# Optimization experiments

Measured on AMD Instinct MI355X. Metric: run time of the kernel, lower is better.

## Reference

```python
import jax, jax.numpy as jnp
import numpy as np

# ---- fixed architecture constants (from init_kwargs) ----
N_WALL, N_ROOF, N_WINDOW = 4, 1, 2
N_RC = N_WALL + N_ROOF
HID = 32
ENC_LEN = 48
DT = 900.0
R_OPAQUE, C_OPAQUE = 10.0, 1.0e5
R_TRANS = 2.0
DIRECT_COEF, ABS_WALL_COEF, ABS_ROOF_COEF = 0.5, 0.5, 0.5
C_ZONE = 1.0e5
B, T = 2048, 1440


def setup_inputs() -> dict:
    key = jax.random.key(0)
    k0, k1, k2 = jax.random.split(key, 3)
    input_X = jax.random.normal(k0, (B, T, 7), dtype=jnp.float32)
    # EnvelopeRC deterministic inits
    rc_R_inv = jnp.concatenate([
        1.0 / (10.0 + 1.0 * jnp.arange(N_WALL, dtype=jnp.float32)),
        1.0 / (20.0 + 2.0 * jnp.arange(N_ROOF, dtype=jnp.float32))])
    rc_C_inv = jnp.concatenate([
        1.0 / (80.0 + 10.0 * jnp.arange(N_WALL, dtype=jnp.float32)),
        1.0 / (60.0 + 10.0 * jnp.arange(N_ROOF, dtype=jnp.float32))])
    window_R_inv = 1.0 / (1.0 + 0.1 * jnp.arange(N_WINDOW, dtype=jnp.float32))
    # Internal MLP: xavier_uniform with gain 0.1, zero bias
    lim1 = 0.1 * np.sqrt(6.0 / (2 + HID))
    int_W1 = jax.random.uniform(k1, (HID, 2), jnp.float32, -lim1, lim1)
    int_b1 = jnp.zeros((HID,), jnp.float32)
    lim2 = 0.1 * np.sqrt(6.0 / (HID + 1))
    int_W2 = jax.random.uniform(k2, (1, HID), jnp.float32, -lim2, lim2)
    int_b2 = jnp.zeros((1,), jnp.float32)
    return {
        'input_X': input_X,
        'rc_R_inv': rc_R_inv, 'rc_C_inv': rc_C_inv, 'window_R_inv': window_R_inv,
        'hvac_gain': jnp.float32(0.1),
        'int_W1': int_W1, 'int_b1': int_b1, 'int_W2': int_W2, 'int_b2': int_b2,
        'int_gain': jnp.float32(0.1),
        'direct_gain': jnp.float32(0.1), 'abs_wall': jnp.float32(0.1), 'abs_roof': jnp.float32(0.1),
        'zone_C_inv': jnp.float32(1.0 / 10000.0),
    }


def _forward(input_X, rc_R_inv, rc_C_inv, window_R_inv, hvac_gain,
             int_W1, int_b1, int_W2, int_b2, int_gain,
             direct_gain, abs_wall, abs_roof, zone_C_inv):
    sp = jax.nn.softplus
    Bn, Tn = input_X.shape[0], input_X.shape[1]
    tz_gt  = input_X[:, :, 0]   # [B,T]
    t_amb  = input_X[:, :, 1]
    sol    = input_X[:, :, 2]
    int_x  = input_X[:, :, 3:6]
    hvac_x = input_X[:, :, 6]

    # Internal MLP (state-free -> vectorized over time)
    h1  = jax.nn.relu(jnp.einsum('bti,hi->bth', int_x[:, :, :2], int_W1) + int_b1)
    sch = jax.nn.sigmoid(jnp.einsum('bth,oh->bto', h1, int_W2) + int_b2)[:, :, 0] + int_x[:, :, 2]
    q_int  = sp(int_gain) * 0.1 * sch          # [B,T]
    q_hvac = sp(hvac_gain) * 0.1 * hvac_x      # [B,T]

    # Bounded RC parameters
    r_inv   = sp(rc_R_inv) * (1.0 / R_OPAQUE)  # [n_rc]
    c_inv   = sp(rc_C_inv) * (1.0 / C_OPAQUE)  # [n_rc]
    win_rsum = jnp.sum(sp(window_R_inv)) * (1.0 / R_TRANS)
    abs_rc  = jnp.where(jnp.arange(N_RC) < N_WALL,
                        sp(abs_wall) * ABS_WALL_COEF,
                        sp(abs_roof) * ABS_ROOF_COEF)   # [n_rc]
    q_dir   = sp(direct_gain) * DIRECT_COEF * sol       # [B,T]
    cz_inv  = sp(zone_C_inv) * (1.0 / C_ZONE)

    # Initial state: Tmid_i = 0.7*Tzone0 + 0.3*Tamb0
    Tz0   = tz_gt[:, 0]                                      # [B]
    Tmid0 = jnp.broadcast_to((0.7 * Tz0 + 0.3 * t_amb[:, 0])[:, None], (Bn, N_RC))

    # Teacher forcing during encoder window: carry GT zone temp while t+1 < enc_len
    tz_gt_next = jnp.concatenate([tz_gt[:, 1:], tz_gt[:, -1:]], axis=1)  # [B,T]
    use_gt = (jnp.arange(Tn) + 1) < ENC_LEN                              # [T]

    xs = (t_amb.T, sol.T, q_dir.T, q_int.T, q_hvac.T, tz_gt_next.T, use_gt)

    def step(carry, x):
        Tz, Tmid = carry                      # [B], [B,n_rc]
        ta, so, qd, qi, qh, gt_next, ug = x
        q_in  = (ta[:, None] - Tmid) * r_inv
        q_out = (Tmid - Tz[:, None]) * r_inv
        dTmid = (q_in - q_out + so[:, None] * abs_rc) * c_inv
        q_env = jnp.sum(q_out, axis=1) + (ta - Tz) * win_rsum
        dTz   = (q_env + qi + qh + qd) * cz_inv
        Tz_new   = Tz + dTz * DT
        Tmid_new = Tmid + dTmid * DT
        Tz_carry = jnp.where(ug, gt_next, Tz_new)
        return (Tz_carry, Tmid_new), Tz_new

    _, tz_seq = jax.lax.scan(step, (Tz0, Tmid0), xs)   # [T,B]
    return jnp.transpose(tz_seq)[:, :, None]           # [B,T,1]


def reference(input_X, rc_R_inv, rc_C_inv, window_R_inv, hvac_gain,
              int_W1, int_b1, int_W2, int_b2, int_gain,
              direct_gain, abs_wall, abs_roof, zone_C_inv):
    return _forward(input_X, rc_R_inv, rc_C_inv, window_R_inv, hvac_gain,
                    int_W1, int_b1, int_W2, int_b2, int_gain,
                    direct_gain, abs_wall, abs_roof, zone_C_inv)
```

## Files before the change

### kernel.cpp

```cpp
#include <hip/hip_runtime.h>
#include <math.h>

#define BATCH 2048
#define TLEN  1440
#define NC    30
#define CL    48

#define E_OFF    0
#define XC_OFF   (E_OFF + NC*6*BATCH)
#define A48_OFF  (XC_OFF + BATCH*NC*6)
#define VCOL_OFF (A48_OFF + 64)
#define PRM_OFF  (VCOL_OFF + 320)
#define WS_FLOATS (PRM_OFF + 32)

__device__ __forceinline__ float sp_precise(float x) { return log1pf(expf(x)); }

struct Prm {
  float P[5], M[5], Q[5], K[5];
  float AZ, dtczw, dtcz, cInt, cHv, cDir;
};
__device__ __forceinline__ Prm make_prm(const float* rcR, const float* rcC,
                                        const float* winR, const float* hvg,
                                        const float* ing, const float* dg,
                                        const float* aw, const float* ar,
                                        const float* zc) {
  Prm p;
  float r[5], cc[5], rsum = 0.f;
  #pragma unroll
  for (int j = 0; j < 5; ++j) {
    r[j] = sp_precise(rcR[j]) * 0.1f;
    cc[j] = sp_precise(rcC[j]) * 1e-5f;
    rsum += r[j];
  }
  float w  = (sp_precise(winR[0]) + sp_precise(winR[1])) * 0.5f;
  float cz = sp_precise(zc[0]) * 1e-5f;
  float aW = sp_precise(aw[0]) * 0.5f, aR = sp_precise(ar[0]) * 0.5f;
  float dtcz = 900.f * cz;
  #pragma unroll
  for (int j = 0; j < 5; ++j) {
    p.P[j] = 900.f * r[j] * cc[j];
    p.M[j] = 1.f - 2.f * p.P[j];
    p.Q[j] = 900.f * cc[j] * ((j < 4) ? aW : aR);
    p.K[j] = dtcz * r[j];
  }
  p.AZ = 1.f - dtcz * (w + rsum);
  p.dtczw = dtcz * w;
  p.dtcz = dtcz;
  p.cInt = sp_precise(ing[0]) * 0.1f;
  p.cHv  = sp_precise(hvg[0]) * 0.1f;
  p.cDir = sp_precise(dg[0])  * 0.5f;
  return p;
}

__global__ void k0_params(const float* __restrict__ rcR, const float* __restrict__ rcC,
                          const float* __restrict__ winR, const float* __restrict__ hvg,
                          const float* __restrict__ ing, const float* __restrict__ dg,
                          const float* __restrict__ aw, const float* __restrict__ ar,
                          const float* __restrict__ zc, float* __restrict__ ws) {
  __shared__ float A0s[36], Ma[36], Mb[36], M16[36], vbuf[2][8];
  int ln = threadIdx.x;
  if (ln == 0) {
    Prm p = make_prm(rcR, rcC, winR, hvg, ing, dg, aw, ar, zc);
    for (int i = 0; i < 36; ++i) A0s[i] = 0.f;
    A0s[0] = p.AZ;
    for (int j = 0; j < 5; ++j) {
      A0s[0 * 6 + 1 + j]       = p.K[j];
      A0s[(1 + j) * 6 + 0]     = p.P[j];
      A0s[(1 + j) * 6 + 1 + j] = p.M[j];
    }
  }
  __syncthreads();
  int i6 = ln / 6, j6 = ln % 6;
  bool act = ln < 36;
#define MM(DST, L, R) { if (act) { float s = 0.f; \
  for (int m = 0; m < 6; ++m) s = fmaf((L)[i6 * 6 + m], (R)[m * 6 + j6], s); \
  (DST)[ln] = s; } __syncthreads(); }
  MM(Mb, A0s, A0s);
  MM(Ma, Mb, Mb);
  MM(Mb, Ma, Ma);
  MM(Ma, Mb, Mb);
  if (act) M16[ln] = Ma[ln];
  __syncthreads();
  MM(Mb, Ma, Ma);
  MM(Ma, Mb, M16);
  if (act) ws[A48_OFF + ln] = Ma[ln];
  if (ln < 6) vbuf[0][ln] = A0s[ln];
  __syncthreads();
  int cur = 0;
  for (int k = 0; k < CL; ++k) {
    if (ln < 6) {
      ws[VCOL_OFF + ln * CL + k] = vbuf[cur][ln];
      float s = 0.f;
      for (int m = 0; m < 6; ++m) s = fmaf(vbuf[cur][m], A0s[m * 6 + ln], s);
      vbuf[1 - cur][ln] = s;
    }
    __syncthreads();
    cur ^= 1;
  }
}

__global__ __launch_bounds__(256) void kb_scan(const float* __restrict__ X,
    const float* __restrict__ rcR, const float* __restrict__ rcC,
    const float* __restrict__ winR, const float* __restrict__ hvg,
    const float* __restrict__ W1, const float* __restrict__ B1,
    const float* __restrict__ W2, const float* __restrict__ B2,
    const float* __restrict__ ing, const float* __restrict__ dg,
    const float* __restrict__ aw, const float* __restrict__ ar,
    const float* __restrict__ zc,
    float* __restrict__ out, float* __restrict__ ws) {
  int tid = blockIdx.x * 256 + threadIdx.x;
  int c = tid >> 11;
  int b = tid & (BATCH - 1);
  Prm p = make_prm(rcR, rcC, winR, hvg, ing, dg, aw, ar, zc);
  float b2 = B2[0];

  float Tz, T0, T1, T2, T3, T4;
  bool isc0 = (c == 0);
  const float* xb = X + ((size_t)b * TLEN + c * CL) * 7;
  if (isc0) {
    float tz0 = xb[0], ta0 = xb[1];
    Tz = tz0;
    float tm = fmaf(0.7f, tz0, 0.3f * ta0);
    T0 = T1 = T2 = T3 = T4 = tm;
  } else {
    Tz = T0 = T1 = T2 = T3 = T4 = 0.f;
  }
  float* op = out + (size_t)b * TLEN + c * CL;
  float ob0 = 0.f, ob1 = 0.f, ob2 = 0.f;
  #pragma unroll 4
  for (int k = 0; k < CL; ++k) {
    const float* x = xb + k * 7;
    float ta = x[1], so = x[2], x3 = x[3], x4 = x[4], x5 = x[5], hv = x[6];
    float acc = b2;
    #pragma unroll
    for (int h = 0; h < 32; ++h) {
      float z = fmaf(W1[2 * h], x3, fmaf(W1[2 * h + 1], x4, B1[h]));
      acc = fmaf(W2[h], fmaxf(z, 0.f), acc);
    }
    float sch = __frcp_rn(1.f + __expf(-acc)) + x5;
    float q = fmaf(p.cInt, sch, fmaf(p.cHv, hv, p.cDir * so));
    float u = fmaf(p.dtczw, ta, p.dtcz * q);
    float d = fmaf(p.K[0], T0, u);
    d = fmaf(p.K[1], T1, d); d = fmaf(p.K[2], T2, d);
    d = fmaf(p.K[3], T3, d); d = fmaf(p.K[4], T4, d);
    float tzn = fmaf(p.AZ, Tz, d);
    T0 = fmaf(p.M[0], T0, fmaf(p.P[0], Tz, fmaf(p.P[0], ta, p.Q[0] * so)));
    T1 = fmaf(p.M[1], T1, fmaf(p.P[1], Tz, fmaf(p.P[1], ta, p.Q[1] * so)));
    T2 = fmaf(p.M[2], T2, fmaf(p.P[2], Tz, fmaf(p.P[2], ta, p.Q[2] * so)));
    T3 = fmaf(p.M[3], T3, fmaf(p.P[3], Tz, fmaf(p.P[3], ta, p.Q[3] * so)));
    T4 = fmaf(p.M[4], T4, fmaf(p.P[4], Tz, fmaf(p.P[4], ta, p.Q[4] * so)));
    int ph = k & 3;
    if (ph == 0) ob0 = tzn;
    else if (ph == 1) ob1 = tzn;
    else if (ph == 2) ob2 = tzn;
    else ((float4*)op)[k >> 2] = make_float4(ob0, ob1, ob2, tzn);
    Tz = (isc0 && k < 47) ? x[7] : tzn;
  }
  float* e = ws + E_OFF + (size_t)c * 6 * BATCH + b;
  e[0] = Tz;
  e[BATCH] = T0; e[2 * BATCH] = T1; e[3 * BATCH] = T2;
  e[4 * BATCH] = T3; e[5 * BATCH] = T4;
}

__global__ __launch_bounds__(256) void k2b_combine(float* __restrict__ ws) {
  int b = blockIdx.x * 256 + threadIdx.x;
  __shared__ float A48s[36];
  if (threadIdx.x < 36) A48s[threadIdx.x] = ws[A48_OFF + threadIdx.x];
  __syncthreads();
  const float* e = ws + E_OFF;
  float Xs[6];
  #pragma unroll
  for (int j = 0; j < 6; ++j) Xs[j] = e[j * BATCH + b];
  float* xc = ws + XC_OFF + (size_t)b * NC * 6;
  for (int c = 1; c < NC; ++c) {
    #pragma unroll
    for (int j = 0; j < 6; ++j) xc[c * 6 + j] = Xs[j];
    if (c < NC - 1) {
      float Y[6];
      #pragma unroll
      for (int i = 0; i < 6; ++i) {
        float s = e[((size_t)c * 6 + i) * BATCH + b];
        #pragma unroll
        for (int m = 0; m < 6; ++m) s = fmaf(A48s[i * 6 + m], Xs[m], s);
        Y[i] = s;
      }
      #pragma unroll
      for (int j = 0; j < 6; ++j) Xs[j] = Y[j];
    }
  }
}

__global__ __launch_bounds__(256) void k2c_correct(float* __restrict__ out,
                                                   const float* __restrict__ ws) {
  __shared__ float V[6 * CL];
  for (int i = threadIdx.x; i < 6 * CL; i += 256) V[i] = ws[VCOL_OFF + i];
  __syncthreads();
  int tid = blockIdx.x * 256 + threadIdx.x;
  int b = tid / (TLEN - CL);
  int tt = tid - b * (TLEN - CL);
  int t = tt + CL;
  int c = t / CL;
  int kk = t - c * CL;
  const float* xc = ws + XC_OFF + ((size_t)b * NC + c) * 6;
  float s = out[(size_t)b * TLEN + t];
  #pragma unroll
  for (int j = 0; j < 6; ++j) s = fmaf(V[j * CL + kk], xc[j], s);
  out[(size_t)b * TLEN + t] = s;
}

__global__ void k_fallback(const float* __restrict__ X,
    const float* __restrict__ rcR, const float* __restrict__ rcC,
    const float* __restrict__ winR, const float* __restrict__ hvg,
    const float* __restrict__ W1, const float* __restrict__ B1,
    const float* __restrict__ W2, const float* __restrict__ B2,
    const float* __restrict__ ing, const float* __restrict__ dg,
    const float* __restrict__ aw, const float* __restrict__ ar,
    const float* __restrict__ zc, float* __restrict__ out) {
  int b = blockIdx.x * 64 + threadIdx.x;
  if (b >= BATCH) return;
  Prm p = make_prm(rcR, rcC, winR, hvg, ing, dg, aw, ar, zc);
  const float* xb = X + (size_t)b * (TLEN * 7);
  float Tz = xb[0];
  float tm = fmaf(0.7f, xb[0], 0.3f * xb[1]);
  float Tm[5] = {tm, tm, tm, tm, tm};
  for (int t = 0; t < TLEN; ++t) {
    const float* x = xb + t * 7;
    float ta = x[1], so = x[2], x3 = x[3], x4 = x[4], x5 = x[5], hv = x[6];
    float acc = B2[0];
    #pragma unroll
    for (int h = 0; h < 32; ++h) {
      float z = fmaf(W1[2 * h], x3, fmaf(W1[2 * h + 1], x4, B1[h]));
      acc = fmaf(W2[h], fmaxf(z, 0.f), acc);
    }
    float sch = __frcp_rn(1.f + __expf(-acc)) + x5;
    float q = fmaf(p.cInt, sch, fmaf(p.cHv, hv, p.cDir * so));
    float u = fmaf(p.dtczw, ta, p.dtcz * q);
    float d = u;
    #pragma unroll
    for (int j = 0; j < 5; ++j) d = fmaf(p.K[j], Tm[j], d);
    float tzn = fmaf(p.AZ, Tz, d);
    #pragma unroll
    for (int j = 0; j < 5; ++j)
      Tm[j] = fmaf(p.M[j], Tm[j], fmaf(p.P[j], Tz, fmaf(p.P[j], ta, p.Q[j] * so)));
    out[(size_t)b * TLEN + t] = tzn;
    Tz = (t < 47) ? x[7] : tzn;
  }
}

extern "C" void kernel_launch(void* const* d_in, const int* in_sizes, int n_in,
                              void* d_out, int out_size, void* d_ws, size_t ws_size,
                              hipStream_t stream) {
  const float* X    = (const float*)d_in[0];
  const float* rcR  = (const float*)d_in[1];
  const float* rcC  = (const float*)d_in[2];
  const float* winR = (const float*)d_in[3];
  const float* hvg  = (const float*)d_in[4];
  const float* W1   = (const float*)d_in[5];
  const float* B1   = (const float*)d_in[6];
  const float* W2   = (const float*)d_in[7];
  const float* B2   = (const float*)d_in[8];
  const float* ing  = (const float*)d_in[9];
  const float* dg   = (const float*)d_in[10];
  const float* aw   = (const float*)d_in[11];
  const float* ar   = (const float*)d_in[12];
  const float* zc   = (const float*)d_in[13];
  float* out = (float*)d_out;
  float* ws  = (float*)d_ws;

  if (ws_size >= (size_t)WS_FLOATS * sizeof(float)) {
    k0_params<<<1, 64, 0, stream>>>(rcR, rcC, winR, hvg, ing, dg, aw, ar, zc, ws);
    kb_scan<<<(BATCH * NC) / 256, 256, 0, stream>>>(X, rcR, rcC, winR, hvg,
                                                    W1, B1, W2, B2, ing, dg, aw, ar, zc,
                                                    out, ws);
    k2b_combine<<<BATCH / 256, 256, 0, stream>>>(ws);
    k2c_correct<<<(BATCH * (TLEN - CL)) / 256, 256, 0, stream>>>(out, ws);
  } else {
    k_fallback<<<BATCH / 64, 64, 0, stream>>>(X, rcR, rcC, winR, hvg, W1, B1, W2, B2,
                                              ing, dg, aw, ar, zc, out);
  }
}
```

Measured before the change: 221.3 us.

## Stage inputs through LDS with coalesced loads and shrink scan chunks

```diff
diff --git a/kernel.cpp b/kernel.cpp
--- a/kernel.cpp
+++ b/kernel.cpp
@@ -3,14 +3,17 @@
 
 #define BATCH 2048
 #define TLEN  1440
-#define NC    30
-#define CL    48
+#define T7    (TLEN * 7)
+#define CL0   48
+#define CL2   16
+#define NCH   88
+#define TREST (TLEN - CL0)
 
 #define E_OFF    0
-#define XC_OFF   (E_OFF + NC*6*BATCH)
-#define A48_OFF  (XC_OFF + BATCH*NC*6)
-#define VCOL_OFF (A48_OFF + 64)
-#define PRM_OFF  (VCOL_OFF + 320)
+#define XC_OFF   (E_OFF + NCH * BATCH * 8)
+#define A16_OFF  (XC_OFF + BATCH * NCH * 8)
+#define V_OFF    (A16_OFF + 64)
+#define PRM_OFF  (V_OFF + 128)
 #define WS_FLOATS (PRM_OFF + 32)
 
 __device__ __forceinline__ float sp_precise(float x) { return log1pf(expf(x)); }
@@ -57,10 +60,16 @@
                           const float* __restrict__ ing, const float* __restrict__ dg,
                           const float* __restrict__ aw, const float* __restrict__ ar,
                           const float* __restrict__ zc, float* __restrict__ ws) {
-  __shared__ float A0s[36], Ma[36], Mb[36], M16[36], vbuf[2][8];
+  __shared__ float A0s[36], Ma[36], Mb[36], vrow[2][8];
   int ln = threadIdx.x;
   if (ln == 0) {
     Prm p = make_prm(rcR, rcC, winR, hvg, ing, dg, aw, ar, zc);
+    float* prm = ws + PRM_OFF;
+    for (int j = 0; j < 5; ++j) {
+      prm[j] = p.P[j]; prm[5 + j] = p.M[j]; prm[10 + j] = p.Q[j]; prm[15 + j] = p.K[j];
+    }
+    prm[20] = p.AZ; prm[21] = p.dtczw; prm[22] = p.dtcz;
+    prm[23] = p.cInt; prm[24] = p.cHv; prm[25] = p.cDir;
     for (int i = 0; i < 36; ++i) A0s[i] = 0.f;
     A0s[0] = p.AZ;
     for (int j = 0; j < 5; ++j) {
@@ -79,133 +88,156 @@
   MM(Ma, Mb, Mb);
   MM(Mb, Ma, Ma);
   MM(Ma, Mb, Mb);
-  if (act) M16[ln] = Ma[ln];
-  __syncthreads();
-  MM(Mb, Ma, Ma);
-  MM(Ma, Mb, M16);
-  if (act) ws[A48_OFF + ln] = Ma[ln];
-  if (ln < 6) vbuf[0][ln] = A0s[ln];
+  if (act) ws[A16_OFF + ln] = Ma[ln];
+  if (ln < 6) vrow[0][ln] = A0s[ln];
   __syncthreads();
   int cur = 0;
-  for (int k = 0; k < CL; ++k) {
+  for (int kk = 0; kk < CL2; ++kk) {
     if (ln < 6) {
-      ws[VCOL_OFF + ln * CL + k] = vbuf[cur][ln];
+      ws[V_OFF + kk * 8 + ln] = vrow[cur][ln];
       float s = 0.f;
-      for (int m = 0; m < 6; ++m) s = fmaf(vbuf[cur][m], A0s[m * 6 + ln], s);
-      vbuf[1 - cur][ln] = s;
+      for (int m = 0; m < 6; ++m) s = fmaf(vrow[cur][m], A0s[m * 6 + ln], s);
+      vrow[1 - cur][ln] = s;
     }
     __syncthreads();
     cur ^= 1;
   }
 }
 
-__global__ __launch_bounds__(256) void kb_scan(const float* __restrict__ X,
-    const float* __restrict__ rcR, const float* __restrict__ rcC,
-    const float* __restrict__ winR, const float* __restrict__ hvg,
+__global__ __launch_bounds__(256) void kb2_scan(const float* __restrict__ X,
     const float* __restrict__ W1, const float* __restrict__ B1,
     const float* __restrict__ W2, const float* __restrict__ B2,
-    const float* __restrict__ ing, const float* __restrict__ dg,
-    const float* __restrict__ aw, const float* __restrict__ ar,
-    const float* __restrict__ zc,
     float* __restrict__ out, float* __restrict__ ws) {
-  int tid = blockIdx.x * 256 + threadIdx.x;
-  int c = tid >> 11;
-  int b = tid & (BATCH - 1);
-  Prm p = make_prm(rcR, rcC, winR, hvg, ing, dg, aw, ar, zc);
+  __shared__ float lds[256 * 29];
+  int c  = blockIdx.x >> 3;
+  int b0 = (blockIdx.x & 7) << 8;
+  int b  = b0 + threadIdx.x;
+  const float* prm = ws + PRM_OFF;
+  float Pa[5], Mm[5], Qa[5], Ka[5];
+  #pragma unroll
+  for (int j = 0; j < 5; ++j) {
+    Pa[j] = prm[j]; Mm[j] = prm[5 + j]; Qa[j] = prm[10 + j]; Ka[j] = prm[15 + j];
+  }
+  float AZ = prm[20], dtczw = prm[21], dtcz = prm[22];
+  float cInt = prm[23], cHv = prm[24], cDir = prm[25];
   float b2 = B2[0];
-
-  float Tz, T0, T1, T2, T3, T4;
   bool isc0 = (c == 0);
-  const float* xb = X + ((size_t)b * TLEN + c * CL) * 7;
-  if (isc0) {
-    float tz0 = xb[0], ta0 = xb[1];
-    Tz = tz0;
-    float tm = fmaf(0.7f, tz0, 0.3f * ta0);
-    T0 = T1 = T2 = T3 = T4 = tm;
-  } else {
-    Tz = T0 = T1 = T2 = T3 = T4 = 0.f;
-  }
-  float* op = out + (size_t)b * TLEN + c * CL;
-  float ob0 = 0.f, ob1 = 0.f, ob2 = 0.f;
-  #pragma unroll 4
-  for (int k = 0; k < CL; ++k) {
-    const float* x = xb + k * 7;
-    float ta = x[1], so = x[2], x3 = x[3], x4 = x[4], x5 = x[5], hv = x[6];
-    float acc = b2;
-    #pragma unroll
-    for (int h = 0; h < 32; ++h) {
-      float z = fmaf(W1[2 * h], x3, fmaf(W1[2 * h + 1], x4, B1[h]));
-      acc = fmaf(W2[h], fmaxf(z, 0.f), acc);
-    }
-    float sch = __frcp_rn(1.f + __expf(-acc)) + x5;
-    float q = fmaf(p.cInt, sch, fmaf(p.cHv, hv, p.cDir * so));
-    float u = fmaf(p.dtczw, ta, p.dtcz * q);
-    float d = fmaf(p.K[0], T0, u);
-    d = fmaf(p.K[1], T1, d); d = fmaf(p.K[2], T2, d);
-    d = fmaf(p.K[3], T3, d); d = fmaf(p.K[4], T4, d);
-    float tzn = fmaf(p.AZ, Tz, d);
-    T0 = fmaf(p.M[0], T0, fmaf(p.P[0], Tz, fmaf(p.P[0], ta, p.Q[0] * so)));
-    T1 = fmaf(p.M[1], T1, fmaf(p.P[1], Tz, fmaf(p.P[1], ta, p.Q[1] * so)));
-    T2 = fmaf(p.M[2], T2, fmaf(p.P[2], Tz, fmaf(p.P[2], ta, p.Q[2] * so)));
-    T3 = fmaf(p.M[3], T3, fmaf(p.P[3], Tz, fmaf(p.P[3], ta, p.Q[3] * so)));
-    T4 = fmaf(p.M[4], T4, fmaf(p.P[4], Tz, fmaf(p.P[4], ta, p.Q[4] * so)));
-    int ph = k & 3;
-    if (ph == 0) ob0 = tzn;
-    else if (ph == 1) ob1 = tzn;
-    else if (ph == 2) ob2 = tzn;
-    else ((float4*)op)[k >> 2] = make_float4(ob0, ob1, ob2, tzn);
-    Tz = (isc0 && k < 47) ? x[7] : tzn;
-  }
-  float* e = ws + E_OFF + (size_t)c * 6 * BATCH + b;
-  e[0] = Tz;
-  e[BATCH] = T0; e[2 * BATCH] = T1; e[3 * BATCH] = T2;
-  e[4 * BATCH] = T3; e[5 * BATCH] = T4;
+  int t0 = isc0 ? 0 : CL0 + (c - 1) * CL2;
+  int NR = isc0 ? (CL0 / 4) : (CL2 / 4);
+  const float* xb = X + (size_t)b * T7;
+  float Tz = 0.f, T0 = 0.f, T1 = 0.f, T2 = 0.f, T3 = 0.f, T4 = 0.f;
+  float* op = out + (size_t)b * TLEN + t0;
+  int j29 = threadIdx.x * 29;
+
+  for (int r = 0; r < NR; ++r) {
+    int t0r = t0 + r * 4;
+    const float* base = X + ((size_t)b0 * TLEN + t0r) * 7;
+    #pragma unroll
+    for (int i = 0; i < 7; ++i) {
+      int F = i * 256 + threadIdx.x;
+      int row = F / 7, q = F - row * 7;
+      float4 v = *(const float4*)(base + (size_t)row * T7 + q * 4);
+      int la = row * 29 + q * 4;
+      lds[la] = v.x; lds[la + 1] = v.y; lds[la + 2] = v.z; lds[la + 3] = v.w;
+    }
+    __syncthreads();
+    if (isc0 && r == 0) {
+      float tz0 = lds[j29], ta0 = lds[j29 + 1];
+      Tz = tz0;
+      T0 = T1 = T2 = T3 = T4 = fmaf(0.7f, tz0, 0.3f * ta0);
+    }
+    float gtb = 0.f;
+    if (isc0 && (r * 4 + 3) < 47) gtb = xb[(size_t)(t0r + 4) * 7];
+    float o0 = 0.f, o1 = 0.f, o2 = 0.f, o3 = 0.f;
+    #pragma unroll
+    for (int s = 0; s < 4; ++s) {
+      const float* x = &lds[j29 + s * 7];
+      float ta = x[1], so = x[2], x3 = x[3], x4v = x[4], x5 = x[5], hv = x[6];
+      float acc = b2;
+      #pragma unroll
+      for (int h = 0; h < 32; ++h) {
+        float z = fmaf(W1[2 * h], x3, fmaf(W1[2 * h + 1], x4v, B1[h]));
+        acc = fmaf(W2[h], fmaxf(z, 0.f), acc);
+      }
+      float sch = __frcp_rn(1.f + __expf(-acc)) + x5;
+      float q = fmaf(cInt, sch, fmaf(cHv, hv, cDir * so));
+      float u = fmaf(dtczw, ta, dtcz * q);
+      float d = fmaf(Ka[0], T0, u);
+      d = fmaf(Ka[1], T1, d); d = fmaf(Ka[2], T2, d);
+      d = fmaf(Ka[3], T3, d); d = fmaf(Ka[4], T4, d);
+      float tzn = fmaf(AZ, Tz, d);
+      T0 = fmaf(Mm[0], T0, fmaf(Pa[0], Tz, fmaf(Pa[0], ta, Qa[0] * so)));
+      T1 = fmaf(Mm[1], T1, fmaf(Pa[1], Tz, fmaf(Pa[1], ta, Qa[1] * so)));
+      T2 = fmaf(Mm[2], T2, fmaf(Pa[2], Tz, fmaf(Pa[2], ta, Qa[2] * so)));
+      T3 = fmaf(Mm[3], T3, fmaf(Pa[3], Tz, fmaf(Pa[3], ta, Qa[3] * so)));
+      T4 = fmaf(Mm[4], T4, fmaf(Pa[4], Tz, fmaf(Pa[4], ta, Qa[4] * so)));
+      if (s == 0) o0 = tzn; else if (s == 1) o1 = tzn;
+      else if (s == 2) o2 = tzn; else o3 = tzn;
+      int k = r * 4 + s;
+      float gt = (s < 3) ? lds[j29 + (s + 1) * 7] : gtb;
+      Tz = (isc0 && k < 47) ? gt : tzn;
+    }
+    *(float4*)(op + r * 4) = make_float4(o0, o1, o2, o3);
+    __syncthreads();
+  }
+  float* e = ws + E_OFF + ((size_t)c * BATCH + b) * 8;
+  *(float4*)e       = make_float4(Tz, T0, T1, T2);
+  *(float4*)(e + 4) = make_float4(T3, T4, 0.f, 0.f);
 }
 
 __global__ __launch_bounds__(256) void k2b_combine(float* __restrict__ ws) {
   int b = blockIdx.x * 256 + threadIdx.x;
-  __shared__ float A48s[36];
-  if (threadIdx.x < 36) A48s[threadIdx.x] = ws[A48_OFF + threadIdx.x];
-  __syncthreads();
+  float A16r[36];
+  #pragma unroll
+  for (int i = 0; i < 36; ++i) A16r[i] = ws[A16_OFF + i];
   const float* e = ws + E_OFF;
-  float Xs[6];
-  #pragma unroll
-  for (int j = 0; j < 6; ++j) Xs[j] = e[j * BATCH + b];
-  float* xc = ws + XC_OFF + (size_t)b * NC * 6;
-  for (int c = 1; c < NC; ++c) {
-    #pragma unroll
-    for (int j = 0; j < 6; ++j) xc[c * 6 + j] = Xs[j];
-    if (c < NC - 1) {
+  float4 h0 = *(const float4*)(e + (size_t)b * 8);
+  float2 h1 = *(const float2*)(e + (size_t)b * 8 + 4);
+  float Xs[6] = {h0.x, h0.y, h0.z, h0.w, h1.x, h1.y};
+  float* xc = ws + XC_OFF + (size_t)b * NCH * 8;
+  float4 q0 = *(const float4*)(e + ((size_t)1 * BATCH + b) * 8);
+  float2 q1 = *(const float2*)(e + ((size_t)1 * BATCH + b) * 8 + 4);
+  for (int cI = 1; cI < NCH; ++cI) {
+    *(float4*)(xc + cI * 8)     = make_float4(Xs[0], Xs[1], Xs[2], Xs[3]);
+    *(float2*)(xc + cI * 8 + 4) = make_float2(Xs[4], Xs[5]);
+    if (cI < NCH - 1) {
+      const float* en = e + ((size_t)(cI + 1) * BATCH + b) * 8;
+      float4 n0 = *(const float4*)en;
+      float2 n1 = *(const float2*)(en + 4);
+      float ecur[6] = {q0.x, q0.y, q0.z, q0.w, q1.x, q1.y};
       float Y[6];
       #pragma unroll
       for (int i = 0; i < 6; ++i) {
-        float s = e[((size_t)c * 6 + i) * BATCH + b];
+        float s = ecur[i];
         #pragma unroll
-        for (int m = 0; m < 6; ++m) s = fmaf(A48s[i * 6 + m], Xs[m], s);
+        for (int m = 0; m < 6; ++m) s = fmaf(A16r[i * 6 + m], Xs[m], s);
         Y[i] = s;
       }
       #pragma unroll
       for (int j = 0; j < 6; ++j) Xs[j] = Y[j];
+      q0 = n0; q1 = n1;
     }
   }
 }
 
 __global__ __launch_bounds__(256) void k2c_correct(float* __restrict__ out,
                                                    const float* __restrict__ ws) {
-  __shared__ float V[6 * CL];
-  for (int i = threadIdx.x; i < 6 * CL; i += 256) V[i] = ws[VCOL_OFF + i];
-  __syncthreads();
   int tid = blockIdx.x * 256 + threadIdx.x;
-  int b = tid / (TLEN - CL);
-  int tt = tid - b * (TLEN - CL);
-  int t = tt + CL;
-  int c = t / CL;
-  int kk = t - c * CL;
-  const float* xc = ws + XC_OFF + ((size_t)b * NC + c) * 6;
-  float s = out[(size_t)b * TLEN + t];
-  #pragma unroll
-  for (int j = 0; j < 6; ++j) s = fmaf(V[j * CL + kk], xc[j], s);
-  out[(size_t)b * TLEN + t] = s;
+  int b  = tid / TREST;
+  int tt = tid - b * TREST;
+  int c  = (tt >> 4) + 1;
+  int kk = tt & 15;
+  const float* xc = ws + XC_OFF + ((size_t)b * NCH + c) * 8;
+  float4 x0 = *(const float4*)xc;
+  float2 x1 = *(const float2*)(xc + 4);
+  const float* v = ws + V_OFF + kk * 8;
+  float4 v0 = *(const float4*)v;
+  float2 v1 = *(const float2*)(v + 4);
+  size_t o = (size_t)b * TLEN + CL0 + tt;
+  float s = out[o];
+  s = fmaf(v0.x, x0.x, s); s = fmaf(v0.y, x0.y, s); s = fmaf(v0.z, x0.z, s);
+  s = fmaf(v0.w, x0.w, s); s = fmaf(v1.x, x1.x, s); s = fmaf(v1.y, x1.y, s);
+  out[o] = s;
 }
 
 __global__ void k_fallback(const float* __restrict__ X,
@@ -219,7 +251,7 @@
   int b = blockIdx.x * 64 + threadIdx.x;
   if (b >= BATCH) return;
   Prm p = make_prm(rcR, rcC, winR, hvg, ing, dg, aw, ar, zc);
-  const float* xb = X + (size_t)b * (TLEN * 7);
+  const float* xb = X + (size_t)b * T7;
   float Tz = xb[0];
   float tm = fmaf(0.7f, xb[0], 0.3f * xb[1]);
   float Tm[5] = {tm, tm, tm, tm, tm};
@@ -269,11 +301,9 @@
 
   if (ws_size >= (size_t)WS_FLOATS * sizeof(float)) {
     k0_params<<<1, 64, 0, stream>>>(rcR, rcC, winR, hvg, ing, dg, aw, ar, zc, ws);
-    kb_scan<<<(BATCH * NC) / 256, 256, 0, stream>>>(X, rcR, rcC, winR, hvg,
-                                                    W1, B1, W2, B2, ing, dg, aw, ar, zc,
-                                                    out, ws);
+    kb2_scan<<<NCH * 8, 256, 0, stream>>>(X, W1, B1, W2, B2, out, ws);
     k2b_combine<<<BATCH / 256, 256, 0, stream>>>(ws);
-    k2c_correct<<<(BATCH * (TLEN - CL)) / 256, 256, 0, stream>>>(out, ws);
+    k2c_correct<<<(BATCH * TREST) / 256, 256, 0, stream>>>(out, ws);
   } else {
     k_fallback<<<BATCH / 64, 64, 0, stream>>>(X, rcR, rcC, winR, hvg, W1, B1, W2, B2,
                                               ing, dg, aw, ar, zc, out);
```

After: 250.2 us. 13.1% more time.
